# Kernel optimization log

Measured on AMD Instinct MI355X. Metric: run time of the kernel, lower is better.

## Reference

```python
import jax, jax.numpy as jnp
import numpy as np

HEADS = 8
DIM_HEAD = 64
SCALE = DIM_HEAD ** -0.5
EPS = 1e-5


def layernorm(t, g, b):
    mu = t.mean(-1, keepdims=True)
    var = ((t - mu) ** 2).mean(-1, keepdims=True)
    return (t - mu) * jax.lax.rsqrt(var + EPS) * g + b


def setup_inputs() -> dict:
    key = jax.random.key(0)
    ks = jax.random.split(key, 12)
    b, n, dim, inner = 2, 2048, 512, HEADS * DIM_HEAD
    s = dim ** -0.5
    return {
        "x": jax.random.normal(ks[0], (b, n, dim), jnp.float32),
        "context": jax.random.normal(ks[1], (b, n, dim), jnp.float32),
        "g_x": jnp.ones((dim,), jnp.float32),
        "b_x": jnp.zeros((dim,), jnp.float32),
        "g_c": jnp.ones((dim,), jnp.float32),
        "b_c": jnp.zeros((dim,), jnp.float32),
        "W_qk": jax.random.normal(ks[2], (dim, inner), jnp.float32) * s,
        "W_cqk": jax.random.normal(ks[3], (dim, inner), jnp.float32) * s,
        "W_v": jax.random.normal(ks[4], (dim, inner), jnp.float32) * s,
        "W_cv": jax.random.normal(ks[5], (dim, inner), jnp.float32) * s,
        "W_out": jax.random.normal(ks[6], (inner, dim), jnp.float32) * s,
        "b_out": jnp.zeros((dim,), jnp.float32),
        "W_cout": jax.random.normal(ks[7], (inner, dim), jnp.float32) * s,
        "b_cout": jnp.zeros((dim,), jnp.float32),
    }


def reference(x, context, g_x, b_x, g_c, b_c, W_qk, W_cqk, W_v, W_cv, W_out, b_out, W_cout, b_cout):
    b, i, _ = x.shape
    j = context.shape[1]
    xn = layernorm(x, g_x, b_x)
    cn = layernorm(context, g_c, b_c)

    def split_heads(t):  # [b, n, h*d] -> [b, h, n, d]
        return t.reshape(t.shape[0], t.shape[1], HEADS, DIM_HEAD).transpose(0, 2, 1, 3)

    qk = split_heads(xn @ W_qk)
    cqk = split_heads(cn @ W_cqk)
    v = split_heads(xn @ W_v)
    cv = split_heads(cn @ W_cv)

    sim = jnp.einsum('bhid,bhjd->bhij', qk, cqk) * SCALE  # [b,h,i,j]
    attn = jax.nn.softmax(sim, axis=-1)           # rows: x attends to context
    context_attn = jax.nn.softmax(sim, axis=-2)   # cols: context attends to x

    out = jnp.einsum('bhij,bhjd->bhid', attn, cv)            # [b,h,i,d]
    context_out = jnp.einsum('bhij,bhid->bhjd', context_attn, v)  # [b,h,j,d]

    def merge_heads(t):  # [b,h,n,d] -> [b,n,h*d]
        return t.transpose(0, 2, 1, 3).reshape(t.shape[0], t.shape[2], HEADS * DIM_HEAD)

    out = merge_heads(out) @ W_out + b_out
    context_out = merge_heads(context_out) @ W_cout + b_cout
    return out, context_out
```

## Files before the change

### kernel.cpp

```cpp
#include <hip/hip_runtime.h>


typedef _Float16 half_t;
typedef __attribute__((ext_vector_type(4))) _Float16 half4v;
typedef __attribute__((ext_vector_type(8))) _Float16 half8v;
typedef __attribute__((ext_vector_type(4))) float floatx4;

#define MFMA16(a, b, c) __builtin_amdgcn_mfma_f32_16x16x32_f16((a), (b), (c), 0, 0, 0)

#if defined(__has_builtin)
#if __has_builtin(__builtin_amdgcn_exp2f)
#define EXP2F(x) __builtin_amdgcn_exp2f(x)
#else
#define EXP2F(x) exp2f(x)
#endif
#else
#define EXP2F(x) exp2f(x)
#endif

__device__ __forceinline__ void gld16(const half_t* g, half_t* l) {
    __builtin_amdgcn_global_load_lds(
        (const __attribute__((address_space(1))) void*)g,
        (__attribute__((address_space(3))) void*)l, 16, 0, 0);
}

__global__ __launch_bounds__(256) void prep_kernel(
    const float* __restrict__ x, const float* __restrict__ ctx,
    const float* __restrict__ gx, const float* __restrict__ bx,
    const float* __restrict__ gc, const float* __restrict__ bc,
    half_t* __restrict__ xn, half_t* __restrict__ cn,
    const float* __restrict__ W0, const float* __restrict__ W1,
    const float* __restrict__ W2, const float* __restrict__ W3,
    const float* __restrict__ W4, const float* __restrict__ W5,
    half_t* __restrict__ Wt)
{
    __shared__ alignas(16) half_t Ts[128][136];
    const int blk = blockIdx.x;
    const int tid = threadIdx.x;
    const int wave = tid >> 6, lane = tid & 63;

    if (blk < 2048) {
        const int row = blk * 4 + wave;
        const float *src, *g, *b;
        half_t* dst;
        if (row < 4096) {
            src = x + (size_t)row * 512; g = gx; b = bx; dst = xn + (size_t)row * 512;
        } else {
            const size_t r = (size_t)(row - 4096);
            src = ctx + r * 512; g = gc; b = bc; dst = cn + r * 512;
        }
        const float4 a0 = *(const float4*)(src + lane * 4);
        const float4 a1 = *(const float4*)(src + 256 + lane * 4);
        float s = a0.x + a0.y + a0.z + a0.w + a1.x + a1.y + a1.z + a1.w;
        float q = a0.x * a0.x + a0.y * a0.y + a0.z * a0.z + a0.w * a0.w +
                  a1.x * a1.x + a1.y * a1.y + a1.z * a1.z + a1.w * a1.w;
#pragma unroll
        for (int m = 1; m < 64; m <<= 1) {
            s += __shfl_xor(s, m);
            q += __shfl_xor(q, m);
        }
        const float mean = s * (1.0f / 512.0f);
        const float var = q * (1.0f / 512.0f) - mean * mean;
        const float rs = rsqrtf(var + 1e-5f);
        const float4 g0 = *(const float4*)(g + lane * 4);
        const float4 g1 = *(const float4*)(g + 256 + lane * 4);
        const float4 b0 = *(const float4*)(b + lane * 4);
        const float4 b1 = *(const float4*)(b + 256 + lane * 4);
        half4v h0, h1;
        h0[0] = (half_t)((a0.x - mean) * rs * g0.x + b0.x);
        h0[1] = (half_t)((a0.y - mean) * rs * g0.y + b0.y);
        h0[2] = (half_t)((a0.z - mean) * rs * g0.z + b0.z);
        h0[3] = (half_t)((a0.w - mean) * rs * g0.w + b0.w);
        h1[0] = (half_t)((a1.x - mean) * rs * g1.x + b1.x);
        h1[1] = (half_t)((a1.y - mean) * rs * g1.y + b1.y);
        h1[2] = (half_t)((a1.z - mean) * rs * g1.z + b1.z);
        h1[3] = (half_t)((a1.w - mean) * rs * g1.w + b1.w);
        *(half4v*)(dst + lane * 4) = h0;
        *(half4v*)(dst + 256 + lane * 4) = h1;
        return;
    }

    const int b2 = blk - 2048;
    const int mat = b2 >> 4, tile = b2 & 15;
    const float* src;
    switch (mat) {
        case 0: src = W0; break;
        case 1: src = W1; break;
        case 2: src = W2; break;
        case 3: src = W3; break;
        case 4: src = W4; break;
        default: src = W5; break;
    }
    const int tr0 = (tile >> 2) * 128;
    const int tc0 = (tile & 3) * 128;
#pragma unroll
    for (int p = 0; p < 16; ++p) {
        const int idx = p * 256 + tid;
        const int r = idx >> 5, c4 = (idx & 31) * 4;
        const float4 w = *(const float4*)(src + (size_t)(tr0 + r) * 512 + tc0 + c4);
        Ts[c4 + 0][r] = (half_t)w.x;
        Ts[c4 + 1][r] = (half_t)w.y;
        Ts[c4 + 2][r] = (half_t)w.z;
        Ts[c4 + 3][r] = (half_t)w.w;
    }
    __syncthreads();
    half_t* dst = Wt + (size_t)mat * 262144;
#pragma unroll
    for (int p = 0; p < 8; ++p) {
        const int idx = p * 256 + tid;
        const int row = idx >> 4, ch = (idx & 15) * 8;
        *(half8v*)(dst + (size_t)(tc0 + row) * 512 + tr0 + ch) = *(const half8v*)&Ts[row][ch];
    }
}

__global__ __launch_bounds__(256) void gemm_in_kernel(
    const half_t* __restrict__ xn, const half_t* __restrict__ cn,
    const half_t* __restrict__ Wt,
    half_t* __restrict__ qk, half_t* __restrict__ v_t,
    half_t* __restrict__ cqk, half_t* __restrict__ cv_t)
{
    const half_t* A; const half_t* B; half_t* O;
    switch (blockIdx.z) {
        case 0:  A = xn; B = Wt;          O = qk;   break;
        case 1:  A = xn; B = Wt + 262144; O = v_t;  break;
        case 2:  A = cn; B = Wt + 524288; O = cqk;  break;
        default: A = cn; B = Wt + 786432; O = cv_t; break;
    }
    const int tr = blockIdx.z & 1;
    const int mt0 = blockIdx.x * 128;
    const int nt0 = blockIdx.y * 128;

    __shared__ alignas(16) half_t As[128 * 64];
    __shared__ alignas(16) half_t Ws[128 * 64];

    const int tid = threadIdx.x;
    const int wave = tid >> 6, lane = tid & 63;
    const int wr = wave >> 1, wc = wave & 1;
    const int q4 = lane >> 4, c = lane & 15;

    int srow[4], scol[4];
#pragma unroll
    for (int p = 0; p < 4; ++p) {
        const int ofs = p * 4096 + wave * 1024 + lane * 16;
        const int row = ofs >> 7;
        const int pc = (ofs >> 4) & 7;
        srow[p] = row;
        scol[p] = (pc ^ (row & 7)) * 8;
    }

    const half_t* P1 = tr ? As : Ws;
    const half_t* P2 = tr ? Ws : As;

    const floatx4 z4 = {0.f, 0.f, 0.f, 0.f};
    floatx4 acc[4][4];
#pragma unroll
    for (int mt = 0; mt < 4; ++mt)
#pragma unroll
        for (int nt = 0; nt < 4; ++nt) acc[mt][nt] = z4;

    for (int kb = 0; kb < 8; ++kb) {
        const int k0 = kb * 64;
#pragma unroll
        for (int p = 0; p < 4; ++p) {
            const int lofs = p * 2048 + wave * 512;
            gld16(A + (size_t)(mt0 + srow[p]) * 512 + k0 + scol[p], As + lofs);
            gld16(B + (size_t)(nt0 + srow[p]) * 512 + k0 + scol[p], Ws + lofs);
        }
        __syncthreads();
#pragma unroll
        for (int kt = 0; kt < 2; ++kt) {
            half8v f1[4], f2[4];
#pragma unroll
            for (int i = 0; i < 4; ++i) {
                const int r1 = wr * 64 + i * 16 + c;
                const int r2 = wc * 64 + i * 16 + c;
                f1[i] = *(const half8v*)&P1[(r1 << 6) + (((kt * 4 + q4) ^ (r1 & 7)) << 3)];
                f2[i] = *(const half8v*)&P2[(r2 << 6) + (((kt * 4 + q4) ^ (r2 & 7)) << 3)];
            }
#pragma unroll
            for (int mt = 0; mt < 4; ++mt)
#pragma unroll
                for (int nt = 0; nt < 4; ++nt)
                    acc[mt][nt] = MFMA16(f1[mt], f2[nt], acc[mt][nt]);
        }
        __syncthreads();
    }

    const int bb = mt0 >> 11;
    const int nnb = mt0 & 2047;
    if (tr) {
#pragma unroll
        for (int mt = 0; mt < 4; ++mt) {
            const int row = nnb + wr * 64 + mt * 16 + q4 * 4;
#pragma unroll
            for (int nt = 0; nt < 4; ++nt) {
                const int col = nt0 + wc * 64 + nt * 16 + c;
                const int h = col >> 6, dd = col & 63;
                half4v pk;
                pk[0] = (half_t)acc[mt][nt][0];
                pk[1] = (half_t)acc[mt][nt][1];
                pk[2] = (half_t)acc[mt][nt][2];
                pk[3] = (half_t)acc[mt][nt][3];
                *(half4v*)(O + ((size_t)(bb * 8 + h) * 64 + dd) * 2048 + row) = pk;
            }
        }
    } else {
#pragma unroll
        for (int mt = 0; mt < 4; ++mt) {
            const int colw = nt0 + wr * 64 + mt * 16 + q4 * 4;
            const int h = colw >> 6, dd = colw & 63;
#pragma unroll
            for (int nt = 0; nt < 4; ++nt) {
                const int row = nnb + wc * 64 + nt * 16 + c;
                half4v pk;
                pk[0] = (half_t)acc[mt][nt][0];
                pk[1] = (half_t)acc[mt][nt][1];
                pk[2] = (half_t)acc[mt][nt][2];
                pk[3] = (half_t)acc[mt][nt][3];
                *(half4v*)(O + ((size_t)(bb * 8 + h) * 2048 + row) * 64 + dd) = pk;
            }
        }
    }
}

__global__ __launch_bounds__(128, 1) void flash_kernel(
    const half_t* __restrict__ qk, const half_t* __restrict__ cqk,
    const half_t* __restrict__ v_t, const half_t* __restrict__ cv_t,
    half_t* __restrict__ out_h, half_t* __restrict__ ctx_out_h)
{
    const int bh = blockIdx.x, it = blockIdx.y, dir = blockIdx.z;
    const half_t* Q  = dir ? cqk : qk;
    const half_t* K  = dir ? qk  : cqk;
    const half_t* VT = dir ? v_t : cv_t;
    half_t* Out = dir ? ctx_out_h : out_h;
    const half_t* Qb = Q + (size_t)bh * (2048 * 64);
    const half_t* Kb = K + (size_t)bh * (2048 * 64);
    const half_t* VTb = VT + (size_t)bh * (64 * 2048);

    __shared__ alignas(16) half_t Ks[128][72];
    __shared__ alignas(16) half_t CVs[64][136];
    __shared__ alignas(16) half_t Ps[128][72];

    const int tid = threadIdx.x;
    const int wave = tid >> 6, lane = tid & 63;
    const int q4 = lane >> 4, c = lane & 15;
    const int rbase = wave * 64;

    half8v onesb;
#pragma unroll
    for (int j = 0; j < 8; ++j) onesb[j] = (c == 0) ? (half_t)1.0f : (half_t)0.0f;

    half8v qf[4][2];
#pragma unroll
    for (int mt = 0; mt < 4; ++mt)
#pragma unroll
        for (int kt = 0; kt < 2; ++kt) {
            half8v v = *(const half8v*)(Qb + (size_t)(it * 128 + rbase + mt * 16 + c) * 64 +
                                        kt * 32 + q4 * 8);
            qf[mt][kt] = v * (half_t)0.18033688f;
        }

    const floatx4 z4 = {0.f, 0.f, 0.f, 0.f};
    floatx4 accT[4][4];
    floatx4 accL[4];
#pragma unroll
    for (int vt = 0; vt < 4; ++vt)
#pragma unroll
        for (int mt = 0; mt < 4; ++mt) accT[vt][mt] = z4;
#pragma unroll
    for (int mt = 0; mt < 4; ++mt) accL[mt] = z4;

    half8v kpre[8], vpre[8];
#pragma unroll
    for (int p = 0; p < 8; ++p) {
        const int cidx = p * 128 + tid;
        kpre[p] = *(const half8v*)(Kb + (size_t)(cidx >> 3) * 64 + (cidx & 7) * 8);
        vpre[p] = *(const half8v*)(VTb + (size_t)(cidx >> 4) * 2048 + (cidx & 15) * 8);
    }

    for (int jt = 0; jt < 16; ++jt) {
        __syncthreads();
#pragma unroll
        for (int p = 0; p < 8; ++p) {
            const int cidx = p * 128 + tid;
            *(half8v*)&Ks[cidx >> 3][(cidx & 7) * 8] = kpre[p];
            *(half8v*)&CVs[cidx >> 4][(cidx & 15) * 8] = vpre[p];
        }
        __syncthreads();
        if (jt < 15) {
            const half_t* Kt = Kb + (size_t)(jt + 1) * 8192;
            const half_t* Vt = VTb + (jt + 1) * 128;
#pragma unroll
            for (int p = 0; p < 8; ++p) {
                const int cidx = p * 128 + tid;
                kpre[p] = *(const half8v*)(Kt + (size_t)(cidx >> 3) * 64 + (cidx & 7) * 8);
                vpre[p] = *(const half8v*)(Vt + (size_t)(cidx >> 4) * 2048 + (cidx & 15) * 8);
            }
        }

#pragma unroll
        for (int ch = 0; ch < 2; ++ch) {
            floatx4 st[4][4];
#pragma unroll
            for (int nl = 0; nl < 4; ++nl) {
                const int nt = ch * 4 + nl;
                const half8v kf0 = *(const half8v*)&Ks[nt * 16 + c][q4 * 8];
                const half8v kf1 = *(const half8v*)&Ks[nt * 16 + c][32 + q4 * 8];
#pragma unroll
                for (int mt = 0; mt < 4; ++mt) {
                    floatx4 t = MFMA16(kf0, qf[mt][0], z4);
                    st[mt][nl] = MFMA16(kf1, qf[mt][1], t);
                }
            }
#pragma unroll
            for (int mt = 0; mt < 4; ++mt)
#pragma unroll
                for (int nl = 0; nl < 4; ++nl) {
                    half4v pk;
#pragma unroll
                    for (int r = 0; r < 4; ++r)
                        pk[r] = (half_t)EXP2F(fminf(st[mt][nl][r], 15.0f));
                    *(half4v*)&Ps[rbase + mt * 16 + c][(ch * 4 + nl) * 16 + q4 * 4] = pk;
                }
#pragma unroll
            for (int ktl = 0; ktl < 2; ++ktl) {
                const int kofs = ch * 64 + ktl * 32 + q4 * 8;
                half8v pf[4];
#pragma unroll
                for (int mt = 0; mt < 4; ++mt)
                    pf[mt] = *(const half8v*)&Ps[rbase + mt * 16 + c][kofs];
#pragma unroll
                for (int vt = 0; vt < 4; ++vt) {
                    const half8v bf = *(const half8v*)&CVs[vt * 16 + c][kofs];
#pragma unroll
                    for (int mt = 0; mt < 4; ++mt)
                        accT[vt][mt] = MFMA16(bf, pf[mt], accT[vt][mt]);
                }
#pragma unroll
                for (int mt = 0; mt < 4; ++mt)
                    accL[mt] = MFMA16(onesb, pf[mt], accL[mt]);
            }
        }
    }

    const size_t ob = (size_t)(bh >> 3) * 2048 * 512 + (size_t)(bh & 7) * 64;
#pragma unroll
    for (int mt = 0; mt < 4; ++mt) {
        const float l = __shfl(accL[mt][0], c);
        const float rl = 1.0f / l;
        const int row = it * 128 + rbase + mt * 16 + c;
#pragma unroll
        for (int vt = 0; vt < 4; ++vt) {
            half4v pk;
            pk[0] = (half_t)(accT[vt][mt][0] * rl);
            pk[1] = (half_t)(accT[vt][mt][1] * rl);
            pk[2] = (half_t)(accT[vt][mt][2] * rl);
            pk[3] = (half_t)(accT[vt][mt][3] * rl);
            *(half4v*)(Out + ob + (size_t)row * 512 + vt * 16 + q4 * 4) = pk;
        }
    }
}

__global__ __launch_bounds__(256) void gemm_out_kernel(
    const half_t* __restrict__ out_h, const half_t* __restrict__ ctx_out_h,
    const half_t* __restrict__ Wt,
    const float* __restrict__ bout, const float* __restrict__ bcout,
    float* __restrict__ dout)
{
    const half_t* A; const half_t* B; const float* bias; float* O;
    if (blockIdx.z == 0) { A = out_h;     B = Wt + 1048576; bias = bout;  O = dout; }
    else                 { A = ctx_out_h; B = Wt + 1310720; bias = bcout; O = dout + 2097152; }

    const int mt0 = blockIdx.x * 64;
    const int nt0 = blockIdx.y * 128;

    __shared__ alignas(16) half_t As[64 * 64];
    __shared__ alignas(16) half_t Ws[128 * 64];

    const int tid = threadIdx.x;
    const int wave = tid >> 6, lane = tid & 63;
    const int wr = wave >> 1, wc = wave & 1;
    const int q4 = lane >> 4, c = lane & 15;

    int srow[4], scol[4];
#pragma unroll
    for (int p = 0; p < 4; ++p) {
        const int ofs = p * 4096 + wave * 1024 + lane * 16;
        const int row = ofs >> 7;
        const int pc = (ofs >> 4) & 7;
        srow[p] = row;
        scol[p] = (pc ^ (row & 7)) * 8;
    }

    const floatx4 z4 = {0.f, 0.f, 0.f, 0.f};
    floatx4 acc[4][2];
#pragma unroll
    for (int mt = 0; mt < 4; ++mt)
#pragma unroll
        for (int nt = 0; nt < 2; ++nt) acc[mt][nt] = z4;

    for (int kb = 0; kb < 8; ++kb) {
        const int k0 = kb * 64;
#pragma unroll
        for (int p = 0; p < 4; ++p) {
            const int lofs = p * 2048 + wave * 512;
            gld16(B + (size_t)(nt0 + srow[p]) * 512 + k0 + scol[p], Ws + lofs);
            if (p < 2)
                gld16(A + (size_t)(mt0 + srow[p]) * 512 + k0 + scol[p], As + lofs);
        }
        __syncthreads();
#pragma unroll
        for (int kt = 0; kt < 2; ++kt) {
            half8v f1[4], f2[2];
#pragma unroll
            for (int i = 0; i < 4; ++i) {
                const int r1 = wr * 64 + i * 16 + c;
                f1[i] = *(const half8v*)&Ws[(r1 << 6) + (((kt * 4 + q4) ^ (r1 & 7)) << 3)];
            }
#pragma unroll
            for (int i = 0; i < 2; ++i) {
                const int r2 = wc * 32 + i * 16 + c;
                f2[i] = *(const half8v*)&As[(r2 << 6) + (((kt * 4 + q4) ^ (r2 & 7)) << 3)];
            }
#pragma unroll
            for (int mt = 0; mt < 4; ++mt)
#pragma unroll
                for (int nt = 0; nt < 2; ++nt)
                    acc[mt][nt] = MFMA16(f1[mt], f2[nt], acc[mt][nt]);
        }
        __syncthreads();
    }

#pragma unroll
    for (int mt = 0; mt < 4; ++mt) {
        const int col = nt0 + wr * 64 + mt * 16 + q4 * 4;
        const float4 bv = *(const float4*)(bias + col);
#pragma unroll
        for (int nt = 0; nt < 2; ++nt) {
            const int row = mt0 + wc * 32 + nt * 16 + c;
            float4 o;
            o.x = acc[mt][nt][0] + bv.x;
            o.y = acc[mt][nt][1] + bv.y;
            o.z = acc[mt][nt][2] + bv.z;
            o.w = acc[mt][nt][3] + bv.w;
            *(float4*)(O + (size_t)row * 512 + col) = o;
        }
    }
}

extern "C" void kernel_launch(void* const* d_in, const int* in_sizes, int n_in,
                              void* d_out, int out_size, void* d_ws, size_t ws_size,
                              hipStream_t stream)
{
    (void)in_sizes; (void)n_in; (void)out_size; (void)ws_size;
    const float* x      = (const float*)d_in[0];
    const float* ctx    = (const float*)d_in[1];
    const float* g_x    = (const float*)d_in[2];
    const float* b_x    = (const float*)d_in[3];
    const float* g_c    = (const float*)d_in[4];
    const float* b_c    = (const float*)d_in[5];
    const float* W_qk   = (const float*)d_in[6];
    const float* W_cqk  = (const float*)d_in[7];
    const float* W_v    = (const float*)d_in[8];
    const float* W_cv   = (const float*)d_in[9];
    const float* W_out  = (const float*)d_in[10];
    const float* b_out  = (const float*)d_in[11];
    const float* W_cout = (const float*)d_in[12];
    const float* b_cout = (const float*)d_in[13];
    float* out = (float*)d_out;

    half_t* ws = (half_t*)d_ws;
    const size_t SEG = 2097152;
    half_t* xn        = ws;
    half_t* cn        = ws + 1 * SEG;
    half_t* qk        = ws + 2 * SEG;
    half_t* cqk       = ws + 3 * SEG;
    half_t* v_t       = ws + 4 * SEG;
    half_t* cv_t      = ws + 5 * SEG;
    half_t* Wt        = ws + 6 * SEG;
    half_t* out_h     = xn;
    half_t* ctx_out_h = cn;

    prep_kernel<<<2144, 256, 0, stream>>>(x, ctx, g_x, b_x, g_c, b_c, xn, cn,
                                          W_qk, W_v, W_cqk, W_cv, W_out, W_cout, Wt);
    gemm_in_kernel<<<dim3(32, 4, 4), 256, 0, stream>>>(xn, cn, Wt, qk, v_t, cqk, cv_t);
    flash_kernel<<<dim3(16, 16, 2), 128, 0, stream>>>(qk, cqk, v_t, cv_t, out_h, ctx_out_h);
    gemm_out_kernel<<<dim3(64, 4, 2), 256, 0, stream>>>(out_h, ctx_out_h, Wt, b_out, b_cout, out);
}
```

Measured before the change: 194.4 us.

## Split flash attention work across 8 waves with async LDS loads and reduction

The flash kernel moves from 2 waves to 8 waves per block. The waves split the key columns for the score/exp stage, and split the key chunk and the head dimension for the PV accumulation. K and V tiles are now loaded straight into LDS with global_load_lds using an XOR swizzle, replacing the register prefetch. Partial accumulators from the two key-half groups are summed through shared memory at the end. This raises per-CU parallelism and lowers register pressure, but it adds more barriers per tile, loses the register-level prefetch overlap, uses a 65KB LDS footprint, and adds a final reduction pass.

New measurement: 220.2 us. 1.13x slower.

```diff
diff --git a/kernel.cpp b/kernel.cpp
--- a/kernel.cpp
+++ b/kernel.cpp
@@ -223,7 +223,7 @@
     }
 }
 
-__global__ __launch_bounds__(128, 1) void flash_kernel(
+__global__ __launch_bounds__(512, 4) void flash_kernel(
     const half_t* __restrict__ qk, const half_t* __restrict__ cqk,
     const half_t* __restrict__ v_t, const half_t* __restrict__ cv_t,
     half_t* __restrict__ out_h, half_t* __restrict__ ctx_out_h)
@@ -237,14 +237,18 @@
     const half_t* Kb = K + (size_t)bh * (2048 * 64);
     const half_t* VTb = VT + (size_t)bh * (64 * 2048);
 
-    __shared__ alignas(16) half_t Ks[128][72];
-    __shared__ alignas(16) half_t CVs[64][136];
-    __shared__ alignas(16) half_t Ps[128][72];
+    __shared__ alignas(16) char smem[66560];
+    half_t* Ks  = (half_t*)smem;
+    half_t* CVs = (half_t*)(smem + 16384);
+    half_t* Ps  = (half_t*)(smem + 32768);
 
     const int tid = threadIdx.x;
     const int wave = tid >> 6, lane = tid & 63;
     const int q4 = lane >> 4, c = lane & 15;
-    const int rbase = wave * 64;
+    const int h = wave >> 2;
+    const int sl = wave & 3;
+    const int jq = (wave >> 1) & 1;
+    const int dh = wave & 1;
 
     half8v onesb;
 #pragma unroll
@@ -255,87 +259,80 @@
     for (int mt = 0; mt < 4; ++mt)
 #pragma unroll
         for (int kt = 0; kt < 2; ++kt) {
-            half8v v = *(const half8v*)(Qb + (size_t)(it * 128 + rbase + mt * 16 + c) * 64 +
+            half8v v = *(const half8v*)(Qb + (size_t)(it * 128 + h * 64 + mt * 16 + c) * 64 +
                                         kt * 32 + q4 * 8);
             qf[mt][kt] = v * (half_t)0.18033688f;
         }
 
     const floatx4 z4 = {0.f, 0.f, 0.f, 0.f};
-    floatx4 accT[4][4];
+    floatx4 accT[2][4];
     floatx4 accL[4];
 #pragma unroll
-    for (int vt = 0; vt < 4; ++vt)
+    for (int vt = 0; vt < 2; ++vt)
 #pragma unroll
         for (int mt = 0; mt < 4; ++mt) accT[vt][mt] = z4;
 #pragma unroll
     for (int mt = 0; mt < 4; ++mt) accL[mt] = z4;
 
-    half8v kpre[8], vpre[8];
-#pragma unroll
-    for (int p = 0; p < 8; ++p) {
-        const int cidx = p * 128 + tid;
-        kpre[p] = *(const half8v*)(Kb + (size_t)(cidx >> 3) * 64 + (cidx & 7) * 8);
-        vpre[p] = *(const half8v*)(VTb + (size_t)(cidx >> 4) * 2048 + (cidx & 15) * 8);
-    }
-
     for (int jt = 0; jt < 16; ++jt) {
         __syncthreads();
-#pragma unroll
-        for (int p = 0; p < 8; ++p) {
-            const int cidx = p * 128 + tid;
-            *(half8v*)&Ks[cidx >> 3][(cidx & 7) * 8] = kpre[p];
-            *(half8v*)&CVs[cidx >> 4][(cidx & 15) * 8] = vpre[p];
-        }
-        __syncthreads();
-        if (jt < 15) {
-            const half_t* Kt = Kb + (size_t)(jt + 1) * 8192;
-            const half_t* Vt = VTb + (jt + 1) * 128;
-#pragma unroll
-            for (int p = 0; p < 8; ++p) {
-                const int cidx = p * 128 + tid;
-                kpre[p] = *(const half8v*)(Kt + (size_t)(cidx >> 3) * 64 + (cidx & 7) * 8);
-                vpre[p] = *(const half8v*)(Vt + (size_t)(cidx >> 4) * 2048 + (cidx & 15) * 8);
-            }
-        }
-
-#pragma unroll
-        for (int ch = 0; ch < 2; ++ch) {
-            floatx4 st[4][4];
-#pragma unroll
-            for (int nl = 0; nl < 4; ++nl) {
-                const int nt = ch * 4 + nl;
-                const half8v kf0 = *(const half8v*)&Ks[nt * 16 + c][q4 * 8];
-                const half8v kf1 = *(const half8v*)&Ks[nt * 16 + c][32 + q4 * 8];
-#pragma unroll
-                for (int mt = 0; mt < 4; ++mt) {
-                    floatx4 t = MFMA16(kf0, qf[mt][0], z4);
-                    st[mt][nl] = MFMA16(kf1, qf[mt][1], t);
-                }
-            }
+        {
+            const half_t* Kt = Kb + (size_t)jt * 8192;
+            const half_t* Vt = VTb + jt * 128;
+#pragma unroll
+            for (int p = 0; p < 2; ++p) {
+                const int idx = p * 512 + tid;
+                const int krow = idx >> 3, kch = idx & 7;
+                gld16(Kt + krow * 64 + ((kch ^ (krow & 7)) * 8),
+                      Ks + (p * 512 + wave * 64) * 8);
+                const int vrow = idx >> 4, vch = idx & 15;
+                gld16(Vt + (size_t)vrow * 2048 + ((vch ^ (vrow & 15)) * 8),
+                      CVs + (p * 512 + wave * 64) * 8);
+            }
+        }
+        __syncthreads();
+
+#pragma unroll
+        for (int nl = 0; nl < 2; ++nl) {
+            const int jrow = sl * 32 + nl * 16 + c;
+            const half8v kf0 = *(const half8v*)&Ks[jrow * 64 + ((q4 ^ (jrow & 7)) * 8)];
+            const half8v kf1 = *(const half8v*)&Ks[jrow * 64 + (((4 + q4) ^ (jrow & 7)) * 8)];
+            floatx4 st[4];
+#pragma unroll
+            for (int mt = 0; mt < 4; ++mt) {
+                floatx4 t = MFMA16(kf0, qf[mt][0], z4);
+                st[mt] = MFMA16(kf1, qf[mt][1], t);
+            }
+#pragma unroll
+            for (int mt = 0; mt < 4; ++mt) {
+                half4v pk;
+#pragma unroll
+                for (int r = 0; r < 4; ++r)
+                    pk[r] = (half_t)EXP2F(fminf(st[mt][r], 15.0f));
+                *(half4v*)&Ps[(h * 64 + mt * 16 + c) * 132 + sl * 32 + nl * 16 + q4 * 4] = pk;
+            }
+        }
+        __syncthreads();
+
+#pragma unroll
+        for (int ktl = 0; ktl < 2; ++ktl) {
+            half8v pf[4], bf[2];
 #pragma unroll
             for (int mt = 0; mt < 4; ++mt)
-#pragma unroll
-                for (int nl = 0; nl < 4; ++nl) {
-                    half4v pk;
-#pragma unroll
-                    for (int r = 0; r < 4; ++r)
-                        pk[r] = (half_t)EXP2F(fminf(st[mt][nl][r], 15.0f));
-                    *(half4v*)&Ps[rbase + mt * 16 + c][(ch * 4 + nl) * 16 + q4 * 4] = pk;
-                }
-#pragma unroll
-            for (int ktl = 0; ktl < 2; ++ktl) {
-                const int kofs = ch * 64 + ktl * 32 + q4 * 8;
-                half8v pf[4];
+                pf[mt] = *(const half8v*)&Ps[(h * 64 + mt * 16 + c) * 132 +
+                                             jq * 64 + ktl * 32 + q4 * 8];
+#pragma unroll
+            for (int vt = 0; vt < 2; ++vt) {
+                const int drow = dh * 32 + vt * 16 + c;
+                bf[vt] = *(const half8v*)&CVs[drow * 128 +
+                                              (((jq * 8 + ktl * 4 + q4) ^ c) * 8)];
+            }
+#pragma unroll
+            for (int vt = 0; vt < 2; ++vt)
 #pragma unroll
                 for (int mt = 0; mt < 4; ++mt)
-                    pf[mt] = *(const half8v*)&Ps[rbase + mt * 16 + c][kofs];
-#pragma unroll
-                for (int vt = 0; vt < 4; ++vt) {
-                    const half8v bf = *(const half8v*)&CVs[vt * 16 + c][kofs];
-#pragma unroll
-                    for (int mt = 0; mt < 4; ++mt)
-                        accT[vt][mt] = MFMA16(bf, pf[mt], accT[vt][mt]);
-                }
+                    accT[vt][mt] = MFMA16(bf[vt], pf[mt], accT[vt][mt]);
+            if (dh == 0) {
 #pragma unroll
                 for (int mt = 0; mt < 4; ++mt)
                     accL[mt] = MFMA16(onesb, pf[mt], accL[mt]);
@@ -343,20 +340,59 @@
         }
     }
 
-    const size_t ob = (size_t)(bh >> 3) * 2048 * 512 + (size_t)(bh & 7) * 64;
-#pragma unroll
-    for (int mt = 0; mt < 4; ++mt) {
-        const float l = __shfl(accL[mt][0], c);
-        const float rl = 1.0f / l;
-        const int row = it * 128 + rbase + mt * 16 + c;
-#pragma unroll
-        for (int vt = 0; vt < 4; ++vt) {
-            half4v pk;
-            pk[0] = (half_t)(accT[vt][mt][0] * rl);
-            pk[1] = (half_t)(accT[vt][mt][1] * rl);
-            pk[2] = (half_t)(accT[vt][mt][2] * rl);
-            pk[3] = (half_t)(accT[vt][mt][3] * rl);
-            *(half4v*)(Out + ob + (size_t)row * 512 + vt * 16 + q4 * 4) = pk;
+    float* red = (float*)smem;
+    __syncthreads();
+    if (jq == 1) {
+        const int slot = h * 2 + dh;
+#pragma unroll
+        for (int vt = 0; vt < 2; ++vt)
+#pragma unroll
+            for (int mt = 0; mt < 4; ++mt)
+                *(floatx4*)&red[slot * 2048 + (vt * 4 + mt) * 256 + lane * 4] = accT[vt][mt];
+        if (dh == 0)
+#pragma unroll
+            for (int mt = 0; mt < 4; ++mt)
+                *(floatx4*)&red[8192 + h * 1024 + mt * 256 + lane * 4] = accL[mt];
+    }
+    __syncthreads();
+    if (jq == 0) {
+        const int slot = h * 2 + dh;
+#pragma unroll
+        for (int vt = 0; vt < 2; ++vt)
+#pragma unroll
+            for (int mt = 0; mt < 4; ++mt) {
+                const floatx4 o = *(const floatx4*)&red[slot * 2048 + (vt * 4 + mt) * 256 + lane * 4];
+                accT[vt][mt] += o;
+            }
+        if (dh == 0)
+#pragma unroll
+            for (int mt = 0; mt < 4; ++mt) {
+                const floatx4 o = *(const floatx4*)&red[8192 + h * 1024 + mt * 256 + lane * 4];
+                accL[mt] += o;
+            }
+    }
+    __syncthreads();
+    if (jq == 0 && dh == 0 && q4 == 0) {
+#pragma unroll
+        for (int mt = 0; mt < 4; ++mt)
+            red[10240 + h * 64 + mt * 16 + c] = accL[mt][0];
+    }
+    __syncthreads();
+    if (jq == 0) {
+        const size_t ob = (size_t)(bh >> 3) * 2048 * 512 + (size_t)(bh & 7) * 64;
+#pragma unroll
+        for (int mt = 0; mt < 4; ++mt) {
+            const float rl = 1.0f / red[10240 + h * 64 + mt * 16 + c];
+            const int row = it * 128 + h * 64 + mt * 16 + c;
+#pragma unroll
+            for (int vt = 0; vt < 2; ++vt) {
+                half4v pk;
+                pk[0] = (half_t)(accT[vt][mt][0] * rl);
+                pk[1] = (half_t)(accT[vt][mt][1] * rl);
+                pk[2] = (half_t)(accT[vt][mt][2] * rl);
+                pk[3] = (half_t)(accT[vt][mt][3] * rl);
+                *(half4v*)(Out + ob + (size_t)row * 512 + dh * 32 + vt * 16 + q4 * 4) = pk;
+            }
         }
     }
 }
@@ -484,6 +520,6 @@
     prep_kernel<<<2144, 256, 0, stream>>>(x, ctx, g_x, b_x, g_c, b_c, xn, cn,
                                           W_qk, W_v, W_cqk, W_cv, W_out, W_cout, Wt);
     gemm_in_kernel<<<dim3(32, 4, 4), 256, 0, stream>>>(xn, cn, Wt, qk, v_t, cqk, cv_t);
-    flash_kernel<<<dim3(16, 16, 2), 128, 0, stream>>>(qk, cqk, v_t, cv_t, out_h, ctx_out_h);
+    flash_kernel<<<dim3(16, 16, 2), 512, 0, stream>>>(qk, cqk, v_t, cv_t, out_h, ctx_out_h);
     gemm_out_kernel<<<dim3(64, 4, 2), 256, 0, stream>>>(out_h, ctx_out_h, Wt, b_out, b_cout, out);
 }
```
